# Optimization experiments

Measured on AMD Instinct MI355X. Metric: run time of the kernel, lower is better.

The kernel has to match this reference:

```python
import jax, jax.numpy as jnp
import numpy as np

N, D = 2048, 1024
H, KV, HD = 16, 4, 64
REPEATS = H // KV
SCALE = HD ** -0.5


def setup_inputs() -> dict:
    key = jax.random.key(0)
    ks = jax.random.split(key, 6)
    x = jax.random.normal(ks[0], (N, D), dtype=jnp.float32)
    # rotary tables: cos/sin of interleaved-pair angles (llama-style view_as_complex)
    pos = jnp.arange(N, dtype=jnp.float32)[:, None]
    inv_freq = 1.0 / (10000.0 ** (jnp.arange(0, HD, 2, dtype=jnp.float32) / HD))
    ang = pos * inv_freq[None, :]  # (N, HD//2)
    freqs_cos = jnp.cos(ang)
    freqs_sin = jnp.sin(ang)
    s = 0.02
    Wq = jax.random.normal(ks[1], (D, H * HD), dtype=jnp.float32) * s
    Wk = jax.random.normal(ks[2], (D, KV * HD), dtype=jnp.float32) * s
    Wv = jax.random.normal(ks[3], (D, KV * HD), dtype=jnp.float32) * s
    Wo = jax.random.normal(ks[4], (H * HD, D), dtype=jnp.float32) * s
    return {"x": x, "freqs_cos": freqs_cos, "freqs_sin": freqs_sin,
            "Wq": Wq, "Wk": Wk, "Wv": Wv, "Wo": Wo}


def _rope(t, cos, sin):
    # t: (N, heads, HD); interleaved complex pairs (even=real, odd=imag)
    tr = t[..., 0::2]
    ti = t[..., 1::2]
    c = cos[:, None, :]
    s = sin[:, None, :]
    out_r = tr * c - ti * s
    out_i = tr * s + ti * c
    return jnp.stack([out_r, out_i], axis=-1).reshape(t.shape)


def reference(x, freqs_cos, freqs_sin, Wq, Wk, Wv, Wo):
    n = x.shape[0]
    xq = (x @ Wq).reshape(n, H, HD)
    xk = (x @ Wk).reshape(n, KV, HD)
    xv = (x @ Wv).reshape(n, KV, HD)
    xq = _rope(xq, freqs_cos, freqs_sin)
    xk = _rope(xk, freqs_cos, freqs_sin)
    # repeat_kv along head dim (GQA)
    k = jnp.repeat(xk, REPEATS, axis=1)  # (n, H, HD)
    v = jnp.repeat(xv, REPEATS, axis=1)
    # memory_efficient_attention with mask=None: full attention over token axis
    scores = jnp.einsum('nhd,mhd->hnm', xq, k) * SCALE
    attn = jax.nn.softmax(scores, axis=-1)
    out = jnp.einsum('hnm,mhd->nhd', attn, v)
    return out.reshape(n, H * HD) @ Wo
```

## Files before the change

### kernel.cpp

```cpp
#include <hip/hip_runtime.h>

#define N_TOK 2048
#define DMODEL 1024
#define NH 16
#define NKV 4
#define HDIM 64
#define SCALE_LOG2E 0.1803368801111204f

typedef __attribute__((ext_vector_type(8))) short short8;
typedef __attribute__((ext_vector_type(4))) float f32x4;
typedef __attribute__((ext_vector_type(16))) float f32x16;
typedef __attribute__((ext_vector_type(2))) int i32x2;
typedef __attribute__((ext_vector_type(4))) unsigned int u32x4;
typedef unsigned short u16;
typedef unsigned int u32;

__device__ __forceinline__ u16 f2bf(float x) {
    u32 u = __float_as_uint(x);
    u += 0x7FFF + ((u >> 16) & 1);
    return (u16)(u >> 16);
}
__device__ __forceinline__ u32 pack2(float a, float b) {
    return (u32)f2bf(a) | ((u32)f2bf(b) << 16);
}
__device__ __forceinline__ u32 pack2t(float a, float b) {
    return __builtin_amdgcn_perm(__float_as_uint(b), __float_as_uint(a), 0x07060302u);
}

__device__ __forceinline__ void gload16(const u16* g, u16* l) {
    __builtin_amdgcn_global_load_lds(
        (const __attribute__((address_space(1))) unsigned int*)g,
        (__attribute__((address_space(3))) unsigned int*)l, 16, 0, 0);
}

__global__ __launch_bounds__(256) void prep(
    const float* __restrict__ Wq, const float* __restrict__ Wk,
    const float* __restrict__ Wv, const float* __restrict__ Wo,
    const float* __restrict__ x,
    u16* __restrict__ Wqt, u16* __restrict__ Wkt, u16* __restrict__ Wvt,
    u16* __restrict__ Wot, u16* __restrict__ xb)
{
    const int z = blockIdx.z;
    const int t = threadIdx.x;
    if (z == 4) {
        size_t base = ((size_t)(blockIdx.y * 16 + blockIdx.x)) * 8192;
#pragma unroll
        for (int i = 0; i < 8; ++i) {
            float4 v = *(const float4*)(x + base + i * 1024 + t * 4);
            uint2 p; p.x = pack2(v.x, v.y); p.y = pack2(v.z, v.w);
            *(uint2*)(xb + base + i * 1024 + t * 4) = p;
        }
        return;
    }
    const float* W; u16* Wt; int NC;
    if      (z == 0) { W = Wq; Wt = Wqt; NC = 1024; }
    else if (z == 1) { W = Wk; Wt = Wkt; NC = 256; }
    else if (z == 2) { W = Wv; Wt = Wvt; NC = 256; }
    else             { W = Wo; Wt = Wot; NC = 1024; }
    const int n0 = blockIdx.x * 64;
    if (n0 >= NC) return;
    const int k0 = blockIdx.y * 64;
    __shared__ float T[64][68];
    const int row = t >> 2, cs = (t & 3) * 16;
#pragma unroll
    for (int i = 0; i < 4; ++i)
        *(float4*)&T[row][cs + i * 4] =
            *(const float4*)(W + (size_t)(k0 + row) * NC + n0 + cs + i * 4);
    __syncthreads();
    const int nl = t >> 2, ks = (t & 3) * 16;
    u32 pk[8];
#pragma unroll
    for (int i = 0; i < 8; ++i)
        pk[i] = pack2(T[ks + 2 * i][nl], T[ks + 2 * i + 1][nl]);
    u16* dst = Wt + (size_t)(n0 + nl) * DMODEL + k0 + ks;
    uint4 w0; w0.x = pk[0]; w0.y = pk[1]; w0.z = pk[2]; w0.w = pk[3];
    uint4 w1; w1.x = pk[4]; w1.y = pk[5]; w1.z = pk[6]; w1.w = pk[7];
    *(uint4*)(dst) = w0;
    *(uint4*)(dst + 8) = w1;
}

__global__ __launch_bounds__(256, 3) void gemm_qkv(
    const u16* __restrict__ A,
    const u16* __restrict__ B0, const u16* __restrict__ B1, const u16* __restrict__ B2,
    u16* __restrict__ D0, u16* __restrict__ D1, u16* __restrict__ FVout,
    const float* __restrict__ fc, const float* __restrict__ fs)
{
    __shared__ u16 As[2][64][64];
    __shared__ u16 Bs[2][64][64];
    const int t = threadIdx.x;
    const int m0 = blockIdx.x * 64;
    const int by = blockIdx.y;

    const u16* Bt; int nl0, ep;
    u16* dbf = nullptr; int dstride = 0; float epsc = 1.f;
    if (by < 16)      { Bt = B0; nl0 = by * 64;        dbf = D0; ep = 1; dstride = 1024;
                        epsc = SCALE_LOG2E; }
    else if (by < 20) { Bt = B1; nl0 = (by - 16) * 64; dbf = D1; ep = 1; dstride = 256; }
    else              { Bt = B2; nl0 = (by - 20) * 64; ep = 2; }

    const int w = t >> 6, lane = t & 63;
    const int quad = lane >> 4, l15 = lane & 15;
    const int wm = (w >> 1) * 32, wn = (w & 1) * 32;
    const int rx = l15 & 7;

    const int sro = w * 16 + (lane >> 3);
    const int sco = ((lane & 7) ^ (lane >> 3)) * 8;
    const u16* ApL = A + (size_t)(m0 + sro) * DMODEL + sco;
    const u16* BpL = Bt + (size_t)(nl0 + sro) * DMODEL + sco;

    f32x4 acc[2][2];
#pragma unroll
    for (int i = 0; i < 2; ++i)
#pragma unroll
        for (int j = 0; j < 2; ++j) acc[i][j] = {0.f, 0.f, 0.f, 0.f};

#pragma unroll
    for (int k = 0; k < 2; ++k) {
        gload16(ApL + k * 8 * DMODEL, &As[0][w * 16 + k * 8][0]);
        gload16(BpL + k * 8 * DMODEL, &Bs[0][w * 16 + k * 8][0]);
    }
    __syncthreads();

    for (int it = 0; it < 16; ++it) {
        const int cur = it & 1;
        if (it + 1 < 16) {
            const int kk = (it + 1) * 64;
#pragma unroll
            for (int k = 0; k < 2; ++k) {
                gload16(ApL + k * 8 * DMODEL + kk, &As[cur ^ 1][w * 16 + k * 8][0]);
                gload16(BpL + k * 8 * DMODEL + kk, &Bs[cur ^ 1][w * 16 + k * 8][0]);
            }
        }
#pragma unroll
        for (int c = 0; c < 2; ++c) {
            short8 af[2], bf[2];
#pragma unroll
            for (int i = 0; i < 2; ++i)
                af[i] = *(const short8*)&As[cur][wm + i * 16 + l15][((4 * c + quad) ^ rx) * 8];
#pragma unroll
            for (int j = 0; j < 2; ++j)
                bf[j] = *(const short8*)&Bs[cur][wn + j * 16 + l15][((4 * c + quad) ^ rx) * 8];
#pragma unroll
            for (int i = 0; i < 2; ++i)
#pragma unroll
                for (int j = 0; j < 2; ++j)
                    acc[i][j] = __builtin_amdgcn_mfma_f32_16x16x32_bf16(af[i], bf[j], acc[i][j], 0, 0, 0);
        }
        __syncthreads();
    }

#pragma unroll
    for (int i = 0; i < 2; ++i)
#pragma unroll
        for (int j = 0; j < 2; ++j) {
            const int cl = nl0 + wn + j * 16 + l15;
            if (ep == 1) {
#pragma unroll
                for (int r4 = 0; r4 < 4; ++r4) {
                    const int r = m0 + wm + i * 16 + quad * 4 + r4;
                    float own = acc[i][j][r4];
                    float other = __shfl_xor(own, 1, 64);
                    const int p = (cl & 63) >> 1;
                    const float c = fc[r * 32 + p] * epsc, s = fs[r * 32 + p] * epsc;
                    float outv = ((cl & 1) == 0) ? (own * c - other * s)
                                                 : (other * s + own * c);
                    dbf[(size_t)r * dstride + cl] = f2bf(outv);
                }
            } else {
                const int rb = m0 + wm + i * 16 + quad * 4;
                const int g = cl >> 6, d = cl & 63;
                const int d2 = d >> 5, dl = d & 31;
                const int keyblk = rb >> 7, kg = (rb >> 5) & 3;
                const int kst = (rb >> 4) & 1, hb = (rb >> 3) & 1, jv = rb & 7;
                size_t idx = ((((((size_t)(g * 16 + keyblk) * 4 + kg) * 2 + kst) * 2 + d2)
                               * 2 + hb) * 32 + dl) * 8 + jv;
                uint2 pk;
                pk.x = pack2(acc[i][j][0], acc[i][j][1]);
                pk.y = pack2(acc[i][j][2], acc[i][j][3]);
                *(uint2*)(FVout + idx) = pk;
            }
        }
}

__global__ __launch_bounds__(256, 2) void gemm_out(
    const u16* __restrict__ A, const u16* __restrict__ Bt, float* __restrict__ Dout)
{
    __shared__ u16 As[2][64][64];
    __shared__ u16 Bs[2][64][64];
    const int t = threadIdx.x;
    const int m0 = blockIdx.x * 64;
    const int nl0 = blockIdx.y * 64;

    const int w = t >> 6, lane = t & 63;
    const int quad = lane >> 4, l15 = lane & 15;
    const int wm = (w >> 1) * 32, wn = (w & 1) * 32;
    const int rx = l15 & 7;

    const int sro = w * 16 + (lane >> 3);
    const int sco = ((lane & 7) ^ (lane >> 3)) * 8;
    const u16* ApL = A + (size_t)(m0 + sro) * DMODEL + sco;
    const u16* BpL = Bt + (size_t)(nl0 + sro) * DMODEL + sco;

    f32x4 acc[2][2];
#pragma unroll
    for (int i = 0; i < 2; ++i)
#pragma unroll
        for (int j = 0; j < 2; ++j) acc[i][j] = {0.f, 0.f, 0.f, 0.f};

#pragma unroll
    for (int k = 0; k < 2; ++k) {
        gload16(ApL + k * 8 * DMODEL, &As[0][w * 16 + k * 8][0]);
        gload16(BpL + k * 8 * DMODEL, &Bs[0][w * 16 + k * 8][0]);
    }
    __syncthreads();

    for (int it = 0; it < 16; ++it) {
        const int cur = it & 1;
        if (it + 1 < 16) {
            const int kk = (it + 1) * 64;
#pragma unroll
            for (int k = 0; k < 2; ++k) {
                gload16(ApL + k * 8 * DMODEL + kk, &As[cur ^ 1][w * 16 + k * 8][0]);
                gload16(BpL + k * 8 * DMODEL + kk, &Bs[cur ^ 1][w * 16 + k * 8][0]);
            }
        }
#pragma unroll
        for (int c = 0; c < 2; ++c) {
            short8 af[2], bf[2];
#pragma unroll
            for (int i = 0; i < 2; ++i)
                af[i] = *(const short8*)&As[cur][wm + i * 16 + l15][((4 * c + quad) ^ rx) * 8];
#pragma unroll
            for (int j = 0; j < 2; ++j)
                bf[j] = *(const short8*)&Bs[cur][wn + j * 16 + l15][((4 * c + quad) ^ rx) * 8];
#pragma unroll
            for (int i = 0; i < 2; ++i)
#pragma unroll
                for (int j = 0; j < 2; ++j)
                    acc[i][j] = __builtin_amdgcn_mfma_f32_16x16x32_bf16(af[i], bf[j], acc[i][j], 0, 0, 0);
        }
        __syncthreads();
    }

#pragma unroll
    for (int i = 0; i < 2; ++i)
#pragma unroll
        for (int j = 0; j < 2; ++j) {
            const int cl = nl0 + wn + j * 16 + l15;
#pragma unroll
            for (int r4 = 0; r4 < 4; ++r4) {
                const int r = m0 + wm + i * 16 + quad * 4 + r4;
                Dout[(size_t)r * 1024 + cl] = acc[i][j][r4];
            }
        }
}

__global__ __launch_bounds__(256, 2) void attn(
    const u16* __restrict__ Qb, const u16* __restrict__ Kb,
    const u16* __restrict__ FV, u16* __restrict__ Ob)
{
    __shared__ u16 Ks[2][2][64][72];

    const int t = threadIdx.x;
    const int n0 = blockIdx.x * 64;
    const int h = blockIdx.y, kvh = h >> 2;
    const int w = t >> 6, lane = t & 63;
    const int hi = lane >> 5, l31 = lane & 31;
    const int qgrp = w & 1, khalf = w >> 1;
    const int srow = t >> 1, ssel = (t & 1) * 32;
    const int khalf_s = srow >> 6, klocal = srow & 63;

    const short8 ones = {(short)0x3F80, (short)0x3F80, (short)0x3F80, (short)0x3F80,
                         (short)0x3F80, (short)0x3F80, (short)0x3F80, (short)0x3F80};

    const u16* qp = Qb + (size_t)(n0 + qgrp * 32 + l31) * (NH * HDIM) + h * HDIM + hi * 8;
    short8 qf[4];
#pragma unroll
    for (int s = 0; s < 4; ++s) qf[s] = *(const short8*)(qp + s * 16);

    const u16* kbase = Kb + (size_t)(khalf_s * 1024 + klocal) * (NKV * HDIM) + kvh * HDIM + ssel;
    const u16* fvb = FV + ((size_t)kvh * 16 * 8192) + (size_t)lane * 8;

    f32x16 o[2], o_l;
#pragma unroll
    for (int d2 = 0; d2 < 2; ++d2)
#pragma unroll
        for (int r = 0; r < 16; ++r) o[d2][r] = 0.f;
#pragma unroll
    for (int r = 0; r < 16; ++r) o_l[r] = 0.f;

#pragma unroll
    for (int c = 0; c < 4; ++c)
        *(uint4*)&Ks[0][khalf_s][klocal][ssel + c * 8] = *(const uint4*)(kbase + c * 8);
    __syncthreads();

    for (int rd = 0; rd < 16; ++rd) {
        const int cur = rd & 1, nxt = cur ^ 1;
        const int rdn = (rd + 1) & 15;
        uint4 kr[4];
#pragma unroll
        for (int c = 0; c < 4; ++c)
            kr[c] = *(const uint4*)(kbase + (size_t)(rdn * 64) * (NKV * HDIM) + c * 8);

        short8 vf[2][2][2];
#pragma unroll
        for (int kg = 0; kg < 2; ++kg) {
            const int kg_global = khalf * 32 + rd * 2 + kg;
            const int keyblk = kg_global >> 2, kgi = kg_global & 3;
#pragma unroll
            for (int s = 0; s < 2; ++s)
#pragma unroll
                for (int d2 = 0; d2 < 2; ++d2)
                    vf[kg][s][d2] = *(const short8*)(fvb +
                        ((((size_t)keyblk * 4 + kgi) * 2 + s) * 2 + d2) * 512);
        }

#pragma unroll
        for (int kg = 0; kg < 2; ++kg) {
            f32x16 sa;
#pragma unroll
            for (int r = 0; r < 16; ++r) sa[r] = 0.f;
            __builtin_amdgcn_s_setprio(1);
#pragma unroll
            for (int s = 0; s < 4; ++s) {
                short8 kf = *(const short8*)&Ks[cur][khalf][kg * 32 + l31][s * 16 + hi * 8];
                sa = __builtin_amdgcn_mfma_f32_32x32x16_bf16(kf, qf[s], sa, 0, 0, 0);
            }
            __builtin_amdgcn_s_setprio(0);
            float p[16];
#pragma unroll
            for (int r = 0; r < 16; ++r) p[r] = __builtin_amdgcn_exp2f(sa[r]);
            const u32 A0 = pack2t(p[0],  p[1]);
            const u32 B0 = pack2t(p[2],  p[3]);
            const u32 C0 = pack2t(p[4],  p[5]);
            const u32 D0 = pack2t(p[6],  p[7]);
            const u32 E0 = pack2t(p[8],  p[9]);
            const u32 F0 = pack2t(p[10], p[11]);
            const u32 G0 = pack2t(p[12], p[13]);
            const u32 H0 = pack2t(p[14], p[15]);
            i32x2 X = __builtin_amdgcn_permlane32_swap((int)A0, (int)C0, false, false);
            i32x2 Y = __builtin_amdgcn_permlane32_swap((int)B0, (int)D0, false, false);
            i32x2 Z = __builtin_amdgcn_permlane32_swap((int)E0, (int)G0, false, false);
            i32x2 U = __builtin_amdgcn_permlane32_swap((int)F0, (int)H0, false, false);
            u32x4 t0 = {(u32)X.x, (u32)Y.x, (u32)X.y, (u32)Y.y};
            u32x4 t1 = {(u32)Z.x, (u32)U.x, (u32)Z.y, (u32)U.y};
            const short8 ap0 = __builtin_bit_cast(short8, t0);
            const short8 ap1 = __builtin_bit_cast(short8, t1);
            __builtin_amdgcn_s_setprio(1);
#pragma unroll
            for (int d2 = 0; d2 < 2; ++d2) {
                o[d2] = __builtin_amdgcn_mfma_f32_32x32x16_bf16(ap0, vf[kg][0][d2], o[d2], 0, 0, 0);
                o[d2] = __builtin_amdgcn_mfma_f32_32x32x16_bf16(ap1, vf[kg][1][d2], o[d2], 0, 0, 0);
            }
            o_l = __builtin_amdgcn_mfma_f32_32x32x16_bf16(ap0, ones, o_l, 0, 0, 0);
            o_l = __builtin_amdgcn_mfma_f32_32x32x16_bf16(ap1, ones, o_l, 0, 0, 0);
            __builtin_amdgcn_s_setprio(0);
        }
#pragma unroll
        for (int c = 0; c < 4; ++c)
            *(uint4*)&Ks[nxt][khalf_s][klocal][ssel + c * 8] = kr[c];
        __syncthreads();
    }

    float* Xf = (float*)&Ks[0][0][0][0];
    if (khalf == 1) {
#pragma unroll
        for (int d2 = 0; d2 < 2; ++d2)
#pragma unroll
            for (int r = 0; r < 16; ++r) {
                const int q32 = (r & 3) + 8 * (r >> 2) + 4 * hi;
                Xf[qgrp * 2048 + q32 * 64 + d2 * 32 + l31] = o[d2][r];
            }
        if (l31 == 0) {
#pragma unroll
            for (int r = 0; r < 16; ++r) {
                const int q32 = (r & 3) + 8 * (r >> 2) + 4 * hi;
                Xf[4096 + qgrp * 32 + q32] = o_l[r];
            }
        }
    }
    __syncthreads();
    if (khalf == 0) {
        float linv[16];
#pragma unroll
        for (int r = 0; r < 16; ++r) {
            const int q32 = (r & 3) + 8 * (r >> 2) + 4 * hi;
            linv[r] = 1.f / (o_l[r] + Xf[4096 + qgrp * 32 + q32]);
        }
#pragma unroll
        for (int d2 = 0; d2 < 2; ++d2)
#pragma unroll
            for (int r = 0; r < 16; ++r) {
                const int q32 = (r & 3) + 8 * (r >> 2) + 4 * hi;
                const float val = o[d2][r] + Xf[qgrp * 2048 + q32 * 64 + d2 * 32 + l31];
                const int qrow = n0 + qgrp * 32 + q32;
                Ob[(size_t)qrow * (NH * HDIM) + h * HDIM + d2 * 32 + l31] = f2bf(val * linv[r]);
            }
    }
}

extern "C" void kernel_launch(void* const* d_in, const int* in_sizes, int n_in,
                              void* d_out, int out_size, void* d_ws, size_t ws_size,
                              hipStream_t stream) {
    const float* x  = (const float*)d_in[0];
    const float* fc = (const float*)d_in[1];
    const float* fs = (const float*)d_in[2];
    const float* Wq = (const float*)d_in[3];
    const float* Wk = (const float*)d_in[4];
    const float* Wv = (const float*)d_in[5];
    const float* Wo = (const float*)d_in[6];
    float* out = (float*)d_out;

    u16* ws  = (u16*)d_ws;
    u16* xb  = ws;
    u16* Wqt = xb  + (size_t)2048 * 1024;
    u16* Wkt = Wqt + (size_t)1024 * 1024;
    u16* Wvt = Wkt + (size_t)256 * 1024;
    u16* Wot = Wvt + (size_t)256 * 1024;
    u16* qb  = Wot + (size_t)1024 * 1024;
    u16* kb  = qb  + (size_t)2048 * 1024;
    u16* fv  = kb  + (size_t)2048 * 256;
    u16* aob = fv  + (size_t)256 * 2048;

    prep<<<dim3(16, 16, 5), dim3(256), 0, stream>>>(Wq, Wk, Wv, Wo, x,
                                                    Wqt, Wkt, Wvt, Wot, xb);
    gemm_qkv<<<dim3(32, 24), dim3(256), 0, stream>>>(xb, Wqt, Wkt, Wvt,
                                                     qb, kb, fv, fc, fs);
    attn<<<dim3(32, 16), dim3(256), 0, stream>>>(qb, kb, fv, aob);
    gemm_out<<<dim3(32, 16), dim3(256), 0, stream>>>(aob, Wot, out);
}
```

Before: 136.1 us.

## Triple-buffer LDS in projection GEMMs with partial vmcnt waits

Both the QKV and output projection GEMMs move from double to triple buffering of the LDS tiles, prefetching two K-steps ahead. The full __syncthreads is replaced by an s_waitcnt vmcnt(4) plus a raw s_barrier, so the loads for the newest tile stay in flight across the barrier. This aims to hide global-to-LDS latency better, at the cost of 50% more shared memory per block, which may reduce occupancy. Correctness relies on the gload16 direct-to-LDS loads being tracked by vmcnt.

```diff
diff --git a/kernel.cpp b/kernel.cpp
--- a/kernel.cpp
+++ b/kernel.cpp
@@ -85,8 +85,8 @@
     u16* __restrict__ D0, u16* __restrict__ D1, u16* __restrict__ FVout,
     const float* __restrict__ fc, const float* __restrict__ fs)
 {
-    __shared__ u16 As[2][64][64];
-    __shared__ u16 Bs[2][64][64];
+    __shared__ u16 As[3][64][64];
+    __shared__ u16 Bs[3][64][64];
     const int t = threadIdx.x;
     const int m0 = blockIdx.x * 64;
     const int by = blockIdx.y;
@@ -119,16 +119,23 @@
         gload16(ApL + k * 8 * DMODEL, &As[0][w * 16 + k * 8][0]);
         gload16(BpL + k * 8 * DMODEL, &Bs[0][w * 16 + k * 8][0]);
     }
-    __syncthreads();
-
+#pragma unroll
+    for (int k = 0; k < 2; ++k) {
+        gload16(ApL + k * 8 * DMODEL + 64, &As[1][w * 16 + k * 8][0]);
+        gload16(BpL + k * 8 * DMODEL + 64, &Bs[1][w * 16 + k * 8][0]);
+    }
+    asm volatile("s_waitcnt vmcnt(4)" ::: "memory");
+    __builtin_amdgcn_sched_barrier(0);
+    __builtin_amdgcn_s_barrier();
+
+    int cb = 0, nb = 1, pb = 2;
     for (int it = 0; it < 16; ++it) {
-        const int cur = it & 1;
-        if (it + 1 < 16) {
-            const int kk = (it + 1) * 64;
+        if (it + 2 < 16) {
+            const int kk = (it + 2) * 64;
 #pragma unroll
             for (int k = 0; k < 2; ++k) {
-                gload16(ApL + k * 8 * DMODEL + kk, &As[cur ^ 1][w * 16 + k * 8][0]);
-                gload16(BpL + k * 8 * DMODEL + kk, &Bs[cur ^ 1][w * 16 + k * 8][0]);
+                gload16(ApL + k * 8 * DMODEL + kk, &As[pb][w * 16 + k * 8][0]);
+                gload16(BpL + k * 8 * DMODEL + kk, &Bs[pb][w * 16 + k * 8][0]);
             }
         }
 #pragma unroll
@@ -136,17 +143,21 @@
             short8 af[2], bf[2];
 #pragma unroll
             for (int i = 0; i < 2; ++i)
-                af[i] = *(const short8*)&As[cur][wm + i * 16 + l15][((4 * c + quad) ^ rx) * 8];
+                af[i] = *(const short8*)&As[cb][wm + i * 16 + l15][((4 * c + quad) ^ rx) * 8];
 #pragma unroll
             for (int j = 0; j < 2; ++j)
-                bf[j] = *(const short8*)&Bs[cur][wn + j * 16 + l15][((4 * c + quad) ^ rx) * 8];
+                bf[j] = *(const short8*)&Bs[cb][wn + j * 16 + l15][((4 * c + quad) ^ rx) * 8];
 #pragma unroll
             for (int i = 0; i < 2; ++i)
 #pragma unroll
                 for (int j = 0; j < 2; ++j)
                     acc[i][j] = __builtin_amdgcn_mfma_f32_16x16x32_bf16(af[i], bf[j], acc[i][j], 0, 0, 0);
         }
-        __syncthreads();
+        if (it + 2 < 16) asm volatile("s_waitcnt vmcnt(4)" ::: "memory");
+        else             asm volatile("s_waitcnt vmcnt(0)" ::: "memory");
+        __builtin_amdgcn_sched_barrier(0);
+        __builtin_amdgcn_s_barrier();
+        const int tmp = cb; cb = nb; nb = pb; pb = tmp;
     }
 
 #pragma unroll
@@ -185,8 +196,8 @@
 __global__ __launch_bounds__(256, 2) void gemm_out(
     const u16* __restrict__ A, const u16* __restrict__ Bt, float* __restrict__ Dout)
 {
-    __shared__ u16 As[2][64][64];
-    __shared__ u16 Bs[2][64][64];
+    __shared__ u16 As[3][64][64];
+    __shared__ u16 Bs[3][64][64];
     const int t = threadIdx.x;
     const int m0 = blockIdx.x * 64;
     const int nl0 = blockIdx.y * 64;
@@ -212,16 +223,23 @@
         gload16(ApL + k * 8 * DMODEL, &As[0][w * 16 + k * 8][0]);
         gload16(BpL + k * 8 * DMODEL, &Bs[0][w * 16 + k * 8][0]);
     }
-    __syncthreads();
-
+#pragma unroll
+    for (int k = 0; k < 2; ++k) {
+        gload16(ApL + k * 8 * DMODEL + 64, &As[1][w * 16 + k * 8][0]);
+        gload16(BpL + k * 8 * DMODEL + 64, &Bs[1][w * 16 + k * 8][0]);
+    }
+    asm volatile("s_waitcnt vmcnt(4)" ::: "memory");
+    __builtin_amdgcn_sched_barrier(0);
+    __builtin_amdgcn_s_barrier();
+
+    int cb = 0, nb = 1, pb = 2;
     for (int it = 0; it < 16; ++it) {
-        const int cur = it & 1;
-        if (it + 1 < 16) {
-            const int kk = (it + 1) * 64;
+        if (it + 2 < 16) {
+            const int kk = (it + 2) * 64;
 #pragma unroll
             for (int k = 0; k < 2; ++k) {
-                gload16(ApL + k * 8 * DMODEL + kk, &As[cur ^ 1][w * 16 + k * 8][0]);
-                gload16(BpL + k * 8 * DMODEL + kk, &Bs[cur ^ 1][w * 16 + k * 8][0]);
+                gload16(ApL + k * 8 * DMODEL + kk, &As[pb][w * 16 + k * 8][0]);
+                gload16(BpL + k * 8 * DMODEL + kk, &Bs[pb][w * 16 + k * 8][0]);
             }
         }
 #pragma unroll
@@ -229,17 +247,21 @@
             short8 af[2], bf[2];
 #pragma unroll
             for (int i = 0; i < 2; ++i)
-                af[i] = *(const short8*)&As[cur][wm + i * 16 + l15][((4 * c + quad) ^ rx) * 8];
+                af[i] = *(const short8*)&As[cb][wm + i * 16 + l15][((4 * c + quad) ^ rx) * 8];
 #pragma unroll
             for (int j = 0; j < 2; ++j)
-                bf[j] = *(const short8*)&Bs[cur][wn + j * 16 + l15][((4 * c + quad) ^ rx) * 8];
+                bf[j] = *(const short8*)&Bs[cb][wn + j * 16 + l15][((4 * c + quad) ^ rx) * 8];
 #pragma unroll
             for (int i = 0; i < 2; ++i)
 #pragma unroll
                 for (int j = 0; j < 2; ++j)
                     acc[i][j] = __builtin_amdgcn_mfma_f32_16x16x32_bf16(af[i], bf[j], acc[i][j], 0, 0, 0);
         }
-        __syncthreads();
+        if (it + 2 < 16) asm volatile("s_waitcnt vmcnt(4)" ::: "memory");
+        else             asm volatile("s_waitcnt vmcnt(0)" ::: "memory");
+        __builtin_amdgcn_sched_barrier(0);
+        __builtin_amdgcn_s_barrier();
+        const int tmp = cb; cb = nb; nb = pb; pb = tmp;
     }
 
 #pragma unroll
```

Measured after the change: 128.7 us. 1.06x faster.
